# Kernel optimization log

Measured on AMD Instinct MI355X. Metric: run time of the kernel, lower is better.

The kernel has to match this reference:

```python
import jax, jax.numpy as jnp
import numpy as np

N_NODES = 50000
N_EDGES = 600000
D_IN = 128
HID = 128
N_SAGE = 2          # num_layers - 1
N_GRAPHS = 512
BN_EPS = 1e-5


def setup_inputs() -> dict:
    key = jax.random.key(0)
    ks = jax.random.split(key, 12)
    s = 1.0 / np.sqrt(HID)
    x = jax.random.normal(ks[0], (N_NODES, D_IN), dtype=jnp.float32)
    edge_index = jax.random.randint(ks[1], (2, N_EDGES), 0, N_NODES, dtype=jnp.int32)
    batch = jnp.sort(jax.random.randint(ks[2], (N_NODES,), 0, N_GRAPHS, dtype=jnp.int32))
    # GIN MLP: Linear(D_IN,HID) -> ReLU -> Linear(HID,HID)
    gin_w1 = jax.random.normal(ks[3], (D_IN, HID), dtype=jnp.float32) * s
    gin_b1 = jnp.zeros((HID,), jnp.float32)
    gin_w2 = jax.random.normal(ks[4], (HID, HID), dtype=jnp.float32) * s
    gin_b2 = jnp.zeros((HID,), jnp.float32)
    # SAGEConv layers: lin_l (neighbors, with bias), lin_r (root, no bias)
    sage_wl = jax.random.normal(ks[5], (N_SAGE, HID, HID), dtype=jnp.float32) * s
    sage_bl = jnp.zeros((N_SAGE, HID), jnp.float32)
    sage_wr = jax.random.normal(ks[6], (N_SAGE, HID, HID), dtype=jnp.float32) * s
    # BatchNorm per layer (3 layers)
    bn_gamma = jnp.ones((1 + N_SAGE, HID), jnp.float32)
    bn_beta = jnp.zeros((1 + N_SAGE, HID), jnp.float32)
    return {"x": x, "edge_index": edge_index, "batch": batch,
            "gin_w1": gin_w1, "gin_b1": gin_b1, "gin_w2": gin_w2, "gin_b2": gin_b2,
            "sage_wl": sage_wl, "sage_bl": sage_bl, "sage_wr": sage_wr,
            "bn_gamma": bn_gamma, "bn_beta": bn_beta}


def _batchnorm(h, gamma, beta):
    # training-mode BN over the node dimension (biased variance, as torch)
    mu = jnp.mean(h, axis=0)
    var = jnp.var(h, axis=0)
    return gamma * (h - mu) * jax.lax.rsqrt(var + BN_EPS) + beta


def reference(x, edge_index, batch, gin_w1, gin_b1, gin_w2, gin_b2,
              sage_wl, sage_bl, sage_wr, bn_gamma, bn_beta):
    n = x.shape[0]
    src, dst = edge_index[0], edge_index[1]

    # ---- Layer 0: GINConv (eps=0): mlp(x + sum_{j->i} x_j) ----
    agg = jax.ops.segment_sum(x[src], dst, num_segments=n)  # [N, D_IN]
    h = x + agg
    h = jax.nn.relu(h @ gin_w1 + gin_b1) @ gin_w2 + gin_b2
    h = jax.nn.relu(_batchnorm(h, bn_gamma[0], bn_beta[0]))
    # dropout is identity (eval mode)

    # degree for mean aggregation (shared across SAGE layers)
    deg = jax.ops.segment_sum(jnp.ones((src.shape[0],), h.dtype), dst, num_segments=n)
    inv_deg = (1.0 / jnp.maximum(deg, 1.0))[:, None]  # [N,1]

    # ---- SAGE layers: lin_l(mean_{j->i} h_j) + lin_r(h_i) ----
    for l in range(N_SAGE):
        neigh = jax.ops.segment_sum(h[src], dst, num_segments=n) * inv_deg
        h = neigh @ sage_wl[l] + sage_bl[l] + h @ sage_wr[l]
        h = jax.nn.relu(_batchnorm(h, bn_gamma[l + 1], bn_beta[l + 1]))

    # ---- global mean pool over batch ids ----
    sums = jax.ops.segment_sum(h, batch, num_segments=N_GRAPHS)  # [G, HID]
    counts = jax.ops.segment_sum(jnp.ones((n,), h.dtype), batch, num_segments=N_GRAPHS)
    return sums / jnp.maximum(counts, 1.0)[:, None]
```

## Files before the change

### kernel.cpp

```cpp
#include <hip/hip_runtime.h>

#define N_NODES 50000
#define N_EDGES 600000
#define HID 128
#define N_GRAPHS 512
#define BN_EPS 1e-5f
#define INV_N (1.0f / 50000.0f)

typedef __attribute__((ext_vector_type(8))) short bf16x8;
typedef __attribute__((ext_vector_type(4))) float f32x4;

__device__ __forceinline__ unsigned short f2b(float f) {
    unsigned u = __float_as_uint(f);
    return (unsigned short)((u + 0x7FFFu + ((u >> 16) & 1u)) >> 16);
}
__device__ __forceinline__ float b2f(unsigned short h) {
    return __uint_as_float(((unsigned)h) << 16);
}

#define CONVX_BLOCKS 6250
#define WCONV_BLOCKS 384
#define DEG_BLOCKS   2344
__global__ __launch_bounds__(256) void prep_kernel(
    const float* __restrict__ x, const float* __restrict__ gw1, const float* __restrict__ gw2,
    const float* __restrict__ swl, const float* __restrict__ swr, const int* __restrict__ dst,
    unsigned short* __restrict__ x16, unsigned short* __restrict__ wt, int* __restrict__ deg)
{
    int b = blockIdx.x;
    int t = threadIdx.x;
    if (b < CONVX_BLOCKS) {
        int gid = b * 256 + t;
        int i = gid >> 5, l = gid & 31;
        if (i >= N_NODES) return;
        int c0 = l * 4;
        float4 v = *(const float4*)(x + (size_t)i * 128 + c0);
        ushort4 o;
        o.x = f2b(v.x); o.y = f2b(v.y); o.z = f2b(v.z); o.w = f2b(v.w);
        *(ushort4*)(x16 + (size_t)i * 128 + c0) = o;
    } else if (b < CONVX_BLOCKS + WCONV_BLOCKS) {
        int gid = (b - CONVX_BLOCKS) * 256 + t;
        int m = gid >> 14;
        int e = gid & 16383;
        int k = e >> 7;
        int n = e & 127;
        const float* src = (m == 0) ? gw1 : (m == 1) ? gw2 : (m == 2) ? swl
                         : (m == 3) ? swr : (m == 4) ? (swl + 16384) : (swr + 16384);
        wt[m * 16384 + n * 128 + k] = f2b(src[k * 128 + n]);
    } else {
        int e = (b - CONVX_BLOCKS - WCONV_BLOCKS) * 256 + t;
        if (e < N_EDGES) atomicAdd(&deg[dst[e]], 1);
    }
}

#define ALLOC_BLOCKS 196
__global__ __launch_bounds__(256) void alloc_kernel(int* __restrict__ cursor,
                                                    int* __restrict__ row_beg,
                                                    float* __restrict__ inv_deg,
                                                    int* __restrict__ total,
                                                    const int* __restrict__ batch,
                                                    int* __restrict__ gstart) {
    if (blockIdx.x >= ALLOC_BLOCKS) {
        int g = (blockIdx.x - ALLOC_BLOCKS) * 256 + threadIdx.x;
        if (g > N_GRAPHS) return;
        int lo = 0, hi = N_NODES;
        while (lo < hi) {
            int mid = (lo + hi) >> 1;
            if (batch[mid] < g) lo = mid + 1; else hi = mid;
        }
        gstart[g] = lo;
        return;
    }
    __shared__ int tmp[256];
    __shared__ int base;
    int i = blockIdx.x * 256 + threadIdx.x;
    int d = (i < N_NODES) ? cursor[i] : 0;
    tmp[threadIdx.x] = d;
    __syncthreads();
#pragma unroll
    for (int off = 1; off < 256; off <<= 1) {
        int v = (threadIdx.x >= off) ? tmp[threadIdx.x - off] : 0;
        __syncthreads();
        tmp[threadIdx.x] += v;
        __syncthreads();
    }
    if (threadIdx.x == 255) base = atomicAdd(total, tmp[255]);
    __syncthreads();
    if (i < N_NODES) {
        int b = base + tmp[threadIdx.x] - d;
        row_beg[i] = b;
        cursor[i] = b;
        inv_deg[i] = 1.0f / fmaxf((float)d, 1.0f);
    }
}

__global__ void csr_fill_kernel(const int* __restrict__ src, const int* __restrict__ dst,
                                int* __restrict__ cursor, unsigned short* __restrict__ csr_src, int nE) {
    int e = blockIdx.x * blockDim.x + threadIdx.x;
    if (e < nE) {
        int pos = atomicAdd(&cursor[dst[e]], 1);
        csr_src[pos] = (unsigned short)src[e];
    }
}

#define IDXCAP 2048
template<bool AFF, bool MEAN, bool HACT>
__global__ __launch_bounds__(256) void aggregate_kernel(
    const unsigned short* __restrict__ feat,
    const int* __restrict__ row_beg, const int* __restrict__ row_end,
    const unsigned short* __restrict__ csr_src,
    const float* __restrict__ stats, const float* __restrict__ gamma,
    const float* __restrict__ beta, const float* __restrict__ inv_deg,
    unsigned short* __restrict__ agg, unsigned short* __restrict__ hact, int n)
{
    __shared__ unsigned short idxbuf[IDXCAP];
    const int t = threadIdx.x;
    const int node0 = blockIdx.x * 16;
    const int node = node0 + (t >> 4);
    const int lane = t & 15;
    const int c0 = lane * 8;

    const int last = (node0 + 15 < n) ? node0 + 15 : n - 1;
    const int ebeg = row_beg[node0];
    const int ecnt = row_end[last] - ebeg;
    const bool lds_ok = (ecnt <= IDXCAP);
    if (lds_ok) {
        for (int i = t; i < ecnt; i += 256) idxbuf[i] = csr_src[ebeg + i];
    }
    __syncthreads();
    if (node >= n) return;

    float cc[8], ss[8];
    if (AFF) {
#pragma unroll
        for (int j = 0; j < 8; j++) {
            int col = c0 + j;
            float mu = stats[col] * INV_N;
            float var = stats[128 + col] * INV_N - mu * mu;
            float rs = rsqrtf(var + BN_EPS);
            float c = gamma[col] * rs;
            cc[j] = c;
            ss[j] = beta[col] - mu * c;
        }
    }

    float a[8];
#pragma unroll
    for (int j = 0; j < 8; j++) a[j] = 0.f;

    const int beg = row_beg[node];
    const int deg = row_end[node] - beg;

    if (lds_ok) {
        const int off = beg - ebeg;
        int e = 0;
        for (; e + 7 < deg; e += 8) {
            int s[8];
#pragma unroll
            for (int u = 0; u < 8; u++) s[u] = idxbuf[off + e + u];
            bf16x8 v[8];
#pragma unroll
            for (int u = 0; u < 8; u++)
                v[u] = *(const bf16x8*)(feat + (size_t)s[u] * 128 + c0);
#pragma unroll
            for (int u = 0; u < 8; u++) {
#pragma unroll
                for (int j = 0; j < 8; j++) {
                    float tv = b2f((unsigned short)v[u][j]);
                    if (AFF) tv = fmaxf(tv * cc[j] + ss[j], 0.f);
                    a[j] += tv;
                }
            }
        }
        for (; e + 3 < deg; e += 4) {
            int s[4];
#pragma unroll
            for (int u = 0; u < 4; u++) s[u] = idxbuf[off + e + u];
            bf16x8 v[4];
#pragma unroll
            for (int u = 0; u < 4; u++)
                v[u] = *(const bf16x8*)(feat + (size_t)s[u] * 128 + c0);
#pragma unroll
            for (int u = 0; u < 4; u++) {
#pragma unroll
                for (int j = 0; j < 8; j++) {
                    float tv = b2f((unsigned short)v[u][j]);
                    if (AFF) tv = fmaxf(tv * cc[j] + ss[j], 0.f);
                    a[j] += tv;
                }
            }
        }
        for (; e < deg; e++) {
            int s0 = idxbuf[off + e];
            bf16x8 v0 = *(const bf16x8*)(feat + (size_t)s0 * 128 + c0);
#pragma unroll
            for (int j = 0; j < 8; j++) {
                float tv = b2f((unsigned short)v0[j]);
                if (AFF) tv = fmaxf(tv * cc[j] + ss[j], 0.f);
                a[j] += tv;
            }
        }
    } else {
        int e = beg, end = beg + deg;
        for (; e + 3 < end; e += 4) {
            int s0 = csr_src[e];
            int s1 = csr_src[e + 1];
            int s2 = csr_src[e + 2];
            int s3 = csr_src[e + 3];
            bf16x8 v0 = *(const bf16x8*)(feat + (size_t)s0 * 128 + c0);
            bf16x8 v1 = *(const bf16x8*)(feat + (size_t)s1 * 128 + c0);
            bf16x8 v2 = *(const bf16x8*)(feat + (size_t)s2 * 128 + c0);
            bf16x8 v3 = *(const bf16x8*)(feat + (size_t)s3 * 128 + c0);
#pragma unroll
            for (int j = 0; j < 8; j++) {
                float t0 = b2f((unsigned short)v0[j]);
                float t1 = b2f((unsigned short)v1[j]);
                float t2 = b2f((unsigned short)v2[j]);
                float t3 = b2f((unsigned short)v3[j]);
                if (AFF) {
                    t0 = fmaxf(t0 * cc[j] + ss[j], 0.f);
                    t1 = fmaxf(t1 * cc[j] + ss[j], 0.f);
                    t2 = fmaxf(t2 * cc[j] + ss[j], 0.f);
                    t3 = fmaxf(t3 * cc[j] + ss[j], 0.f);
                }
                a[j] += (t0 + t1) + (t2 + t3);
            }
        }
        for (; e < end; e++) {
            int s0 = csr_src[e];
            bf16x8 v0 = *(const bf16x8*)(feat + (size_t)s0 * 128 + c0);
#pragma unroll
            for (int j = 0; j < 8; j++) {
                float t0 = b2f((unsigned short)v0[j]);
                if (AFF) t0 = fmaxf(t0 * cc[j] + ss[j], 0.f);
                a[j] += t0;
            }
        }
    }

    if (MEAN) {
        float s = inv_deg[node];
#pragma unroll
        for (int j = 0; j < 8; j++) a[j] *= s;
    }
    bf16x8 o;
#pragma unroll
    for (int j = 0; j < 8; j++) o[j] = (short)f2b(a[j]);
    *(bf16x8*)(agg + (size_t)node * 128 + c0) = o;

    if (HACT) {
        bf16x8 v = *(const bf16x8*)(feat + (size_t)node * 128 + c0);
        bf16x8 h;
#pragma unroll
        for (int j = 0; j < 8; j++)
            h[j] = (short)f2b(fmaxf(b2f((unsigned short)v[j]) * cc[j] + ss[j], 0.f));
        *(bf16x8*)(hact + (size_t)node * 128 + c0) = h;
    }
}

__global__ __launch_bounds__(256, 2) void gemm_gin_kernel(
    const unsigned short* __restrict__ X, const unsigned short* __restrict__ AGG,
    const unsigned short* __restrict__ W1t, const unsigned short* __restrict__ W2t,
    const float* __restrict__ b1, const float* __restrict__ b2,
    float* __restrict__ stats, unsigned short* __restrict__ Cb,
    int M, int ntiles)
{
    __shared__ unsigned short t1[32][136];
    __shared__ float red[2][128];

    const int t = threadIdx.x;
    const int wave = t >> 6;
    const int lane = t & 63;
    const int colhalf = wave & 1;
    const int rowpair = wave >> 1;
    const int m16 = lane & 15;
    const int quad = lane >> 4;
    const int k0 = quad * 8;
    const int colbase = colhalf * 64;
    const int lrow = rowpair * 16 + m16;

    const bf16x8 zero8 = {0, 0, 0, 0, 0, 0, 0, 0};

    bf16x8 w1f[4][4], w2f[4][4];
#pragma unroll
    for (int ct = 0; ct < 4; ct++) {
        int col = colbase + ct * 16 + m16;
#pragma unroll
        for (int kc = 0; kc < 4; kc++) {
            w1f[ct][kc] = *(const bf16x8*)(W1t + (size_t)col * 128 + kc * 32 + k0);
            w2f[ct][kc] = *(const bf16x8*)(W2t + (size_t)col * 128 + kc * 32 + k0);
        }
    }
    f32x4 bs1[4], bs2[4];
#pragma unroll
    for (int ct = 0; ct < 4; ct++) {
        bs1[ct] = *(const f32x4*)(b1 + colbase + ct * 16 + quad * 4);
        bs2[ct] = *(const f32x4*)(b2 + colbase + ct * 16 + quad * 4);
    }

    float psum[4][4], psq[4][4];
#pragma unroll
    for (int ct = 0; ct < 4; ct++)
#pragma unroll
        for (int r = 0; r < 4; r++) { psum[ct][r] = 0.f; psq[ct][r] = 0.f; }

    for (int tile = blockIdx.x; tile < ntiles; tile += gridDim.x) {
        int arow = tile * 32 + rowpair * 16 + m16;
        bool aok = arow < M;

        bf16x8 a[4];
#pragma unroll
        for (int kc = 0; kc < 4; kc++) {
            if (aok) {
                bf16x8 vx = *(const bf16x8*)(X + (size_t)arow * 128 + kc * 32 + k0);
                bf16x8 vg = *(const bf16x8*)(AGG + (size_t)arow * 128 + kc * 32 + k0);
                bf16x8 r;
#pragma unroll
                for (int i = 0; i < 8; i++)
                    r[i] = (short)f2b(b2f((unsigned short)vx[i]) + b2f((unsigned short)vg[i]));
                a[kc] = r;
            } else {
                a[kc] = zero8;
            }
        }

        f32x4 acc[4];
#pragma unroll
        for (int ct = 0; ct < 4; ct++) acc[ct] = (f32x4){0.f, 0.f, 0.f, 0.f};
#pragma unroll
        for (int kc = 0; kc < 4; kc++)
#pragma unroll
            for (int ct = 0; ct < 4; ct++)
                acc[ct] = __builtin_amdgcn_mfma_f32_16x16x32_bf16(w1f[ct][kc], a[kc], acc[ct], 0, 0, 0);

        __syncthreads();
#pragma unroll
        for (int ct = 0; ct < 4; ct++) {
            f32x4 v = acc[ct] + bs1[ct];
            ushort4 o;
            o.x = f2b(fmaxf(v[0], 0.f));
            o.y = f2b(fmaxf(v[1], 0.f));
            o.z = f2b(fmaxf(v[2], 0.f));
            o.w = f2b(fmaxf(v[3], 0.f));
            *(ushort4*)&t1[lrow][colbase + ct * 16 + quad * 4] = o;
        }
        __syncthreads();

        bf16x8 ta[4];
#pragma unroll
        for (int kc = 0; kc < 4; kc++)
            ta[kc] = *(const bf16x8*)&t1[lrow][kc * 32 + k0];

        f32x4 acc2[4];
#pragma unroll
        for (int ct = 0; ct < 4; ct++) acc2[ct] = (f32x4){0.f, 0.f, 0.f, 0.f};
#pragma unroll
        for (int kc = 0; kc < 4; kc++)
#pragma unroll
            for (int ct = 0; ct < 4; ct++)
                acc2[ct] = __builtin_amdgcn_mfma_f32_16x16x32_bf16(w2f[ct][kc], ta[kc], acc2[ct], 0, 0, 0);

        int orow = arow;
        if (orow < M) {
#pragma unroll
            for (int ct = 0; ct < 4; ct++) {
                f32x4 v = acc2[ct] + bs2[ct];
                int col = colbase + ct * 16 + quad * 4;
#pragma unroll
                for (int r = 0; r < 4; r++) { psum[ct][r] += v[r]; psq[ct][r] += v[r] * v[r]; }
                ushort4 o;
                o.x = f2b(v[0]); o.y = f2b(v[1]); o.z = f2b(v[2]); o.w = f2b(v[3]);
                *(ushort4*)(Cb + (size_t)orow * 128 + col) = o;
            }
        }
    }

#pragma unroll
    for (int ct = 0; ct < 4; ct++)
#pragma unroll
        for (int r = 0; r < 4; r++) {
#pragma unroll
            for (int mask = 1; mask <= 8; mask <<= 1) {
                psum[ct][r] += __shfl_xor(psum[ct][r], mask, 64);
                psq[ct][r]  += __shfl_xor(psq[ct][r], mask, 64);
            }
        }
    __syncthreads();
    if (m16 == 0) {
#pragma unroll
        for (int ct = 0; ct < 4; ct++)
#pragma unroll
            for (int r = 0; r < 4; r++)
                red[rowpair][colbase + ct * 16 + quad * 4 + r] = psum[ct][r];
    }
    __syncthreads();
    if (t < 128) atomicAdd(&stats[t], red[0][t] + red[1][t]);
    __syncthreads();
    if (m16 == 0) {
#pragma unroll
        for (int ct = 0; ct < 4; ct++)
#pragma unroll
            for (int r = 0; r < 4; r++)
                red[rowpair][colbase + ct * 16 + quad * 4 + r] = psq[ct][r];
    }
    __syncthreads();
    if (t < 128) atomicAdd(&stats[128 + t], red[0][t] + red[1][t]);
}

__global__ __launch_bounds__(256) void gemm_dual_kernel(
    const unsigned short* __restrict__ A1, const unsigned short* __restrict__ A2,
    const unsigned short* __restrict__ W1t, const unsigned short* __restrict__ W2t,
    const float* __restrict__ bias, float* __restrict__ stats,
    unsigned short* __restrict__ Cb, int M, int ntiles)
{
    __shared__ float red[128];

    const int t = threadIdx.x;
    const int wave = t >> 6;
    const int lane = t & 63;
    const int m16 = lane & 15;
    const int quad = lane >> 4;
    const int k0 = quad * 8;
    const int colbase = wave * 32;

    const bf16x8 zero8 = {0, 0, 0, 0, 0, 0, 0, 0};

    bf16x8 w1f[2][4], w2f[2][4];
#pragma unroll
    for (int ct = 0; ct < 2; ct++) {
        int col = colbase + ct * 16 + m16;
#pragma unroll
        for (int kc = 0; kc < 4; kc++) {
            w1f[ct][kc] = *(const bf16x8*)(W1t + (size_t)col * 128 + kc * 32 + k0);
            w2f[ct][kc] = *(const bf16x8*)(W2t + (size_t)col * 128 + kc * 32 + k0);
        }
    }
    f32x4 bs[2];
#pragma unroll
    for (int ct = 0; ct < 2; ct++)
        bs[ct] = *(const f32x4*)(bias + colbase + ct * 16 + quad * 4);

    float psum[2][4], psq[2][4];
#pragma unroll
    for (int ct = 0; ct < 2; ct++)
#pragma unroll
        for (int r = 0; r < 4; r++) { psum[ct][r] = 0.f; psq[ct][r] = 0.f; }

    bf16x8 a1[4], a2[4], a1n[4], a2n[4];

    int tile = blockIdx.x;
    if (tile < ntiles) {
        int arow = tile * 16 + m16;
        bool aok = arow < M;
#pragma unroll
        for (int kc = 0; kc < 4; kc++) {
            a1[kc] = aok ? *(const bf16x8*)(A1 + (size_t)arow * 128 + kc * 32 + k0) : zero8;
            a2[kc] = aok ? *(const bf16x8*)(A2 + (size_t)arow * 128 + kc * 32 + k0) : zero8;
        }
    }

    for (; tile < ntiles; tile += gridDim.x) {
        int nt = tile + gridDim.x;
        if (nt < ntiles) {
            int arow = nt * 16 + m16;
            bool aok = arow < M;
#pragma unroll
            for (int kc = 0; kc < 4; kc++) {
                a1n[kc] = aok ? *(const bf16x8*)(A1 + (size_t)arow * 128 + kc * 32 + k0) : zero8;
                a2n[kc] = aok ? *(const bf16x8*)(A2 + (size_t)arow * 128 + kc * 32 + k0) : zero8;
            }
        }

        f32x4 acc[2];
        acc[0] = (f32x4){0.f, 0.f, 0.f, 0.f};
        acc[1] = (f32x4){0.f, 0.f, 0.f, 0.f};
#pragma unroll
        for (int kc = 0; kc < 4; kc++) {
#pragma unroll
            for (int ct = 0; ct < 2; ct++) {
                acc[ct] = __builtin_amdgcn_mfma_f32_16x16x32_bf16(w1f[ct][kc], a1[kc], acc[ct], 0, 0, 0);
                acc[ct] = __builtin_amdgcn_mfma_f32_16x16x32_bf16(w2f[ct][kc], a2[kc], acc[ct], 0, 0, 0);
            }
        }

        int orow = tile * 16 + m16;
        if (orow < M) {
#pragma unroll
            for (int ct = 0; ct < 2; ct++) {
                f32x4 v = acc[ct] + bs[ct];
                int col = colbase + ct * 16 + quad * 4;
#pragma unroll
                for (int r = 0; r < 4; r++) { psum[ct][r] += v[r]; psq[ct][r] += v[r] * v[r]; }
                ushort4 o;
                o.x = f2b(v[0]); o.y = f2b(v[1]); o.z = f2b(v[2]); o.w = f2b(v[3]);
                *(ushort4*)(Cb + (size_t)orow * 128 + col) = o;
            }
        }

        if (nt < ntiles) {
            a1[0] = a1n[0]; a1[1] = a1n[1]; a1[2] = a1n[2]; a1[3] = a1n[3];
            a2[0] = a2n[0]; a2[1] = a2n[1]; a2[2] = a2n[2]; a2[3] = a2n[3];
        }
    }

#pragma unroll
    for (int ct = 0; ct < 2; ct++)
#pragma unroll
        for (int r = 0; r < 4; r++) {
#pragma unroll
            for (int mask = 1; mask <= 8; mask <<= 1) {
                psum[ct][r] += __shfl_xor(psum[ct][r], mask, 64);
                psq[ct][r]  += __shfl_xor(psq[ct][r], mask, 64);
            }
        }
    if (m16 == 0) {
#pragma unroll
        for (int ct = 0; ct < 2; ct++)
#pragma unroll
            for (int r = 0; r < 4; r++)
                red[colbase + ct * 16 + quad * 4 + r] = psum[ct][r];
    }
    __syncthreads();
    if (t < 128) atomicAdd(&stats[t], red[t]);
    __syncthreads();
    if (m16 == 0) {
#pragma unroll
        for (int ct = 0; ct < 2; ct++)
#pragma unroll
            for (int r = 0; r < 4; r++)
                red[colbase + ct * 16 + quad * 4 + r] = psq[ct][r];
    }
    __syncthreads();
    if (t < 128) atomicAdd(&stats[128 + t], red[t]);
}

__global__ __launch_bounds__(128) void pool_mean_kernel(const unsigned short* __restrict__ h,
                                                        const int* __restrict__ gstart,
                                                        const float* __restrict__ stats,
                                                        const float* __restrict__ gamma,
                                                        const float* __restrict__ beta,
                                                        float* __restrict__ out) {
    __shared__ float red[8][128];
    int g = blockIdx.x;
    int t = threadIdx.x;
    int lane = t & 15, grp = t >> 4;
    int c0 = lane * 8;
    float c[8], b[8];
#pragma unroll
    for (int j = 0; j < 8; j++) {
        int col = c0 + j;
        float mu = stats[col] * INV_N;
        float var = stats[128 + col] * INV_N - mu * mu;
        float rs = rsqrtf(var + BN_EPS);
        c[j] = gamma[col] * rs;
        b[j] = beta[col] - mu * c[j];
    }
    int beg = gstart[g];
    int end = gstart[g + 1];
    float s[8];
#pragma unroll
    for (int j = 0; j < 8; j++) s[j] = 0.f;
    for (int i = beg + grp; i < end; i += 8) {
        bf16x8 v = *(const bf16x8*)(h + (size_t)i * 128 + c0);
#pragma unroll
        for (int j = 0; j < 8; j++)
            s[j] += fmaxf(b2f((unsigned short)v[j]) * c[j] + b[j], 0.f);
    }
#pragma unroll
    for (int j = 0; j < 8; j++) red[grp][c0 + j] = s[j];
    __syncthreads();
    if (t < 16) {
        float cnt = fmaxf((float)(end - beg), 1.0f);
        int cc0 = t * 8;
#pragma unroll
        for (int j = 0; j < 8; j++) {
            float tot = 0.f;
#pragma unroll
            for (int r = 0; r < 8; r++) tot += red[r][cc0 + j];
            out[(size_t)g * 128 + cc0 + j] = tot / cnt;
        }
    }
}

extern "C" void kernel_launch(void* const* d_in, const int* in_sizes, int n_in,
                              void* d_out, int out_size, void* d_ws, size_t ws_size,
                              hipStream_t stream) {
    const float* x    = (const float*)d_in[0];
    const int*   ei   = (const int*)d_in[1];
    const int*   src  = ei;
    const int*   dst  = ei + N_EDGES;
    const int*   batch = (const int*)d_in[2];
    const float* gw1  = (const float*)d_in[3];
    const float* gb1  = (const float*)d_in[4];
    const float* gw2  = (const float*)d_in[5];
    const float* gb2  = (const float*)d_in[6];
    const float* swl  = (const float*)d_in[7];
    const float* sbl  = (const float*)d_in[8];
    const float* swr  = (const float*)d_in[9];
    const float* bng  = (const float*)d_in[10];
    const float* bnb  = (const float*)d_in[11];
    float* out = (float*)d_out;

    float* ws = (float*)d_ws;
    unsigned short* x16    = (unsigned short*)(ws + 0);
    unsigned short* agg16  = (unsigned short*)(ws + 3200000);
    unsigned short* hact16 = (unsigned short*)(ws + 6400000);
    unsigned short* hpre16 = (unsigned short*)(ws + 9600000);
    unsigned short* wt     = (unsigned short*)(ws + 12800000);
    float*          inv_deg= ws + 12850000;
    int*            row_beg= (int*)(ws + 12900000);
    int*            cursor = (int*)(ws + 12950000);
    int*            total  = cursor + 50000;
    float*          stats  = (float*)(cursor + 50001);
    unsigned short* csr_src= (unsigned short*)(ws + 13100000);
    int*            gstart = (int*)(ws + 13700000);

    const int aggr_blocks = (N_NODES + 15) / 16;
    const int ntiles32 = (N_NODES + 31) / 32;
    const int ntiles16 = (N_NODES + 15) / 16;
    const int ggrid = 512;

    hipMemsetAsync(cursor, 0, (50001 + 768) * sizeof(int), stream);

    prep_kernel<<<CONVX_BLOCKS + WCONV_BLOCKS + DEG_BLOCKS, 256, 0, stream>>>(
        x, gw1, gw2, swl, swr, dst, x16, wt, cursor);

    alloc_kernel<<<ALLOC_BLOCKS + 3, 256, 0, stream>>>(cursor, row_beg, inv_deg, total, batch, gstart);
    csr_fill_kernel<<<(N_EDGES + 255) / 256, 256, 0, stream>>>(src, dst, cursor, csr_src, N_EDGES);

    aggregate_kernel<false, false, false><<<aggr_blocks, 256, 0, stream>>>(
        x16, row_beg, cursor, csr_src, nullptr, nullptr, nullptr, nullptr, agg16, nullptr, N_NODES);
    gemm_gin_kernel<<<ggrid, 256, 0, stream>>>(
        x16, agg16, wt + 0 * 16384, wt + 1 * 16384, gb1, gb2, stats + 0, hpre16, N_NODES, ntiles32);

    aggregate_kernel<true, true, true><<<aggr_blocks, 256, 0, stream>>>(
        hpre16, row_beg, cursor, csr_src, stats + 0, bng + 0 * HID, bnb + 0 * HID, inv_deg,
        agg16, hact16, N_NODES);
    gemm_dual_kernel<<<ggrid, 256, 0, stream>>>(
        agg16, hact16, wt + 2 * 16384, wt + 3 * 16384, sbl + 0 * HID, stats + 256, hpre16, N_NODES, ntiles16);

    aggregate_kernel<true, true, true><<<aggr_blocks, 256, 0, stream>>>(
        hpre16, row_beg, cursor, csr_src, stats + 256, bng + 1 * HID, bnb + 1 * HID, inv_deg,
        agg16, hact16, N_NODES);
    gemm_dual_kernel<<<ggrid, 256, 0, stream>>>(
        agg16, hact16, wt + 4 * 16384, wt + 5 * 16384, sbl + 1 * HID, stats + 512, hpre16, N_NODES, ntiles16);

    pool_mean_kernel<<<N_GRAPHS, 128, 0, stream>>>(
        hpre16, gstart, stats + 512, bng + 2 * HID, bnb + 2 * HID, out);
}
```

Baseline: 348.9 us.

## Store features in column-sliced layout and gather per slice for cache locality

Feature matrices are rearranged into 8 column slices of 16 bf16 each (slice-major), and the aggregation becomes a per-slice gather kernel so each block's working set (one 1.6MB slice) fits in L2. BN+ReLU application is moved out of the gather into a separate elementwise finish kernel that writes activated features once. BN stats atomics are spread across 8 partial copies to reduce contention. This adds two extra kernel launches and an extra full read/write pass per layer in exchange for better gather cache reuse.

```diff
diff --git a/kernel.cpp b/kernel.cpp
--- a/kernel.cpp
+++ b/kernel.cpp
@@ -6,6 +6,9 @@
 #define N_GRAPHS 512
 #define BN_EPS 1e-5f
 #define INV_N (1.0f / 50000.0f)
+#define SLICE_STRIDE 800000
+#define GATHER_GROUPS 391
+#define IDXCAP 4096
 
 typedef __attribute__((ext_vector_type(8))) short bf16x8;
 typedef __attribute__((ext_vector_type(4))) float f32x4;
@@ -16,6 +19,13 @@
 }
 __device__ __forceinline__ float b2f(unsigned short h) {
     return __uint_as_float(((unsigned)h) << 16);
+}
+
+__device__ __forceinline__ float stats_sum(const float* __restrict__ s, int idx) {
+    float v = 0.f;
+#pragma unroll
+    for (int r = 0; r < 8; r++) v += s[r * 256 + idx];
+    return v;
 }
 
 #define CONVX_BLOCKS 6250
@@ -36,7 +46,7 @@
         float4 v = *(const float4*)(x + (size_t)i * 128 + c0);
         ushort4 o;
         o.x = f2b(v.x); o.y = f2b(v.y); o.z = f2b(v.z); o.w = f2b(v.w);
-        *(ushort4*)(x16 + (size_t)i * 128 + c0) = o;
+        *(ushort4*)(x16 + (size_t)(l >> 2) * SLICE_STRIDE + (size_t)i * 16 + (l & 3) * 4) = o;
     } else if (b < CONVX_BLOCKS + WCONV_BLOCKS) {
         int gid = (b - CONVX_BLOCKS) * 256 + t;
         int m = gid >> 14;
@@ -102,53 +112,38 @@
     }
 }
 
-#define IDXCAP 2048
-template<bool AFF, bool MEAN, bool HACT>
-__global__ __launch_bounds__(256) void aggregate_kernel(
-    const unsigned short* __restrict__ feat,
+template<bool MEAN>
+__global__ __launch_bounds__(256) void gather_slice_kernel(
+    const unsigned short* __restrict__ feat_s,
     const int* __restrict__ row_beg, const int* __restrict__ row_end,
     const unsigned short* __restrict__ csr_src,
-    const float* __restrict__ stats, const float* __restrict__ gamma,
-    const float* __restrict__ beta, const float* __restrict__ inv_deg,
-    unsigned short* __restrict__ agg, unsigned short* __restrict__ hact, int n)
+    const float* __restrict__ inv_deg,
+    unsigned short* __restrict__ out_s)
 {
     __shared__ unsigned short idxbuf[IDXCAP];
     const int t = threadIdx.x;
-    const int node0 = blockIdx.x * 16;
-    const int node = node0 + (t >> 4);
-    const int lane = t & 15;
-    const int c0 = lane * 8;
-
-    const int last = (node0 + 15 < n) ? node0 + 15 : n - 1;
+    const int slice = blockIdx.x & 7;
+    const int grp = blockIdx.x >> 3;
+    const int node0 = grp * 128;
+    const int nlast = (node0 + 127 < N_NODES) ? node0 + 127 : N_NODES - 1;
+    const int node = node0 + (t >> 1);
+    const int l8 = (t & 1) * 8;
+    const unsigned short* fbase = feat_s + (size_t)slice * SLICE_STRIDE + l8;
+
     const int ebeg = row_beg[node0];
-    const int ecnt = row_end[last] - ebeg;
+    const int ecnt = row_end[nlast] - ebeg;
     const bool lds_ok = (ecnt <= IDXCAP);
-    if (lds_ok) {
+    if (lds_ok)
         for (int i = t; i < ecnt; i += 256) idxbuf[i] = csr_src[ebeg + i];
-    }
-    __syncthreads();
-    if (node >= n) return;
-
-    float cc[8], ss[8];
-    if (AFF) {
-#pragma unroll
-        for (int j = 0; j < 8; j++) {
-            int col = c0 + j;
-            float mu = stats[col] * INV_N;
-            float var = stats[128 + col] * INV_N - mu * mu;
-            float rs = rsqrtf(var + BN_EPS);
-            float c = gamma[col] * rs;
-            cc[j] = c;
-            ss[j] = beta[col] - mu * c;
-        }
-    }
-
-    float a[8];
-#pragma unroll
-    for (int j = 0; j < 8; j++) a[j] = 0.f;
+    __syncthreads();
+    if (node >= N_NODES) return;
 
     const int beg = row_beg[node];
     const int deg = row_end[node] - beg;
+
+    float a[8];
+#pragma unroll
+    for (int j = 0; j < 8; j++) a[j] = 0.f;
 
     if (lds_ok) {
         const int off = beg - ebeg;
@@ -160,16 +155,12 @@
             bf16x8 v[8];
 #pragma unroll
             for (int u = 0; u < 8; u++)
-                v[u] = *(const bf16x8*)(feat + (size_t)s[u] * 128 + c0);
-#pragma unroll
-            for (int u = 0; u < 8; u++) {
-#pragma unroll
-                for (int j = 0; j < 8; j++) {
-                    float tv = b2f((unsigned short)v[u][j]);
-                    if (AFF) tv = fmaxf(tv * cc[j] + ss[j], 0.f);
-                    a[j] += tv;
-                }
-            }
+                v[u] = *(const bf16x8*)(fbase + (size_t)s[u] * 16);
+#pragma unroll
+            for (int u = 0; u < 8; u++)
+#pragma unroll
+                for (int j = 0; j < 8; j++)
+                    a[j] += b2f((unsigned short)v[u][j]);
         }
         for (; e + 3 < deg; e += 4) {
             int s[4];
@@ -178,83 +169,39 @@
             bf16x8 v[4];
 #pragma unroll
             for (int u = 0; u < 4; u++)
-                v[u] = *(const bf16x8*)(feat + (size_t)s[u] * 128 + c0);
-#pragma unroll
-            for (int u = 0; u < 4; u++) {
-#pragma unroll
-                for (int j = 0; j < 8; j++) {
-                    float tv = b2f((unsigned short)v[u][j]);
-                    if (AFF) tv = fmaxf(tv * cc[j] + ss[j], 0.f);
-                    a[j] += tv;
-                }
-            }
+                v[u] = *(const bf16x8*)(fbase + (size_t)s[u] * 16);
+#pragma unroll
+            for (int u = 0; u < 4; u++)
+#pragma unroll
+                for (int j = 0; j < 8; j++)
+                    a[j] += b2f((unsigned short)v[u][j]);
         }
         for (; e < deg; e++) {
             int s0 = idxbuf[off + e];
-            bf16x8 v0 = *(const bf16x8*)(feat + (size_t)s0 * 128 + c0);
-#pragma unroll
-            for (int j = 0; j < 8; j++) {
-                float tv = b2f((unsigned short)v0[j]);
-                if (AFF) tv = fmaxf(tv * cc[j] + ss[j], 0.f);
-                a[j] += tv;
-            }
+            bf16x8 v0 = *(const bf16x8*)(fbase + (size_t)s0 * 16);
+#pragma unroll
+            for (int j = 0; j < 8; j++)
+                a[j] += b2f((unsigned short)v0[j]);
         }
     } else {
-        int e = beg, end = beg + deg;
-        for (; e + 3 < end; e += 4) {
+        for (int e = beg; e < beg + deg; e++) {
             int s0 = csr_src[e];
-            int s1 = csr_src[e + 1];
-            int s2 = csr_src[e + 2];
-            int s3 = csr_src[e + 3];
-            bf16x8 v0 = *(const bf16x8*)(feat + (size_t)s0 * 128 + c0);
-            bf16x8 v1 = *(const bf16x8*)(feat + (size_t)s1 * 128 + c0);
-            bf16x8 v2 = *(const bf16x8*)(feat + (size_t)s2 * 128 + c0);
-            bf16x8 v3 = *(const bf16x8*)(feat + (size_t)s3 * 128 + c0);
-#pragma unroll
-            for (int j = 0; j < 8; j++) {
-                float t0 = b2f((unsigned short)v0[j]);
-                float t1 = b2f((unsigned short)v1[j]);
-                float t2 = b2f((unsigned short)v2[j]);
-                float t3 = b2f((unsigned short)v3[j]);
-                if (AFF) {
-                    t0 = fmaxf(t0 * cc[j] + ss[j], 0.f);
-                    t1 = fmaxf(t1 * cc[j] + ss[j], 0.f);
-                    t2 = fmaxf(t2 * cc[j] + ss[j], 0.f);
-                    t3 = fmaxf(t3 * cc[j] + ss[j], 0.f);
-                }
-                a[j] += (t0 + t1) + (t2 + t3);
-            }
-        }
-        for (; e < end; e++) {
-            int s0 = csr_src[e];
-            bf16x8 v0 = *(const bf16x8*)(feat + (size_t)s0 * 128 + c0);
-#pragma unroll
-            for (int j = 0; j < 8; j++) {
-                float t0 = b2f((unsigned short)v0[j]);
-                if (AFF) t0 = fmaxf(t0 * cc[j] + ss[j], 0.f);
-                a[j] += t0;
-            }
+            bf16x8 v0 = *(const bf16x8*)(fbase + (size_t)s0 * 16);
+#pragma unroll
+            for (int j = 0; j < 8; j++)
+                a[j] += b2f((unsigned short)v0[j]);
         }
     }
 
     if (MEAN) {
-        float s = inv_deg[node];
-#pragma unroll
-        for (int j = 0; j < 8; j++) a[j] *= s;
+        float sc = inv_deg[node];
+#pragma unroll
+        for (int j = 0; j < 8; j++) a[j] *= sc;
     }
     bf16x8 o;
 #pragma unroll
     for (int j = 0; j < 8; j++) o[j] = (short)f2b(a[j]);
-    *(bf16x8*)(agg + (size_t)node * 128 + c0) = o;
-
-    if (HACT) {
-        bf16x8 v = *(const bf16x8*)(feat + (size_t)node * 128 + c0);
-        bf16x8 h;
-#pragma unroll
-        for (int j = 0; j < 8; j++)
-            h[j] = (short)f2b(fmaxf(b2f((unsigned short)v[j]) * cc[j] + ss[j], 0.f));
-        *(bf16x8*)(hact + (size_t)node * 128 + c0) = h;
-    }
+    *(bf16x8*)(out_s + (size_t)slice * SLICE_STRIDE + (size_t)node * 16 + l8) = o;
 }
 
 __global__ __launch_bounds__(256, 2) void gemm_gin_kernel(
@@ -311,8 +258,10 @@
 #pragma unroll
         for (int kc = 0; kc < 4; kc++) {
             if (aok) {
-                bf16x8 vx = *(const bf16x8*)(X + (size_t)arow * 128 + kc * 32 + k0);
-                bf16x8 vg = *(const bf16x8*)(AGG + (size_t)arow * 128 + kc * 32 + k0);
+                size_t aoff = (size_t)(kc * 2 + (quad >> 1)) * SLICE_STRIDE
+                            + (size_t)arow * 16 + (quad & 1) * 8;
+                bf16x8 vx = *(const bf16x8*)(X + aoff);
+                bf16x8 vg = *(const bf16x8*)(AGG + aoff);
                 bf16x8 r;
 #pragma unroll
                 for (int i = 0; i < 8; i++)
@@ -359,17 +308,16 @@
             for (int ct = 0; ct < 4; ct++)
                 acc2[ct] = __builtin_amdgcn_mfma_f32_16x16x32_bf16(w2f[ct][kc], ta[kc], acc2[ct], 0, 0, 0);
 
-        int orow = arow;
-        if (orow < M) {
+        if (arow < M) {
 #pragma unroll
             for (int ct = 0; ct < 4; ct++) {
                 f32x4 v = acc2[ct] + bs2[ct];
-                int col = colbase + ct * 16 + quad * 4;
 #pragma unroll
                 for (int r = 0; r < 4; r++) { psum[ct][r] += v[r]; psq[ct][r] += v[r] * v[r]; }
                 ushort4 o;
                 o.x = f2b(v[0]); o.y = f2b(v[1]); o.z = f2b(v[2]); o.w = f2b(v[3]);
-                *(ushort4*)(Cb + (size_t)orow * 128 + col) = o;
+                int cs = (colbase >> 4) + ct;
+                *(ushort4*)(Cb + (size_t)cs * SLICE_STRIDE + (size_t)arow * 16 + quad * 4) = o;
             }
         }
     }
@@ -393,7 +341,7 @@
                 red[rowpair][colbase + ct * 16 + quad * 4 + r] = psum[ct][r];
     }
     __syncthreads();
-    if (t < 128) atomicAdd(&stats[t], red[0][t] + red[1][t]);
+    if (t < 128) atomicAdd(&stats[(blockIdx.x & 7) * 256 + t], red[0][t] + red[1][t]);
     __syncthreads();
     if (m16 == 0) {
 #pragma unroll
@@ -403,7 +351,7 @@
                 red[rowpair][colbase + ct * 16 + quad * 4 + r] = psq[ct][r];
     }
     __syncthreads();
-    if (t < 128) atomicAdd(&stats[128 + t], red[0][t] + red[1][t]);
+    if (t < 128) atomicAdd(&stats[(blockIdx.x & 7) * 256 + 128 + t], red[0][t] + red[1][t]);
 }
 
 __global__ __launch_bounds__(256) void gemm_dual_kernel(
@@ -453,8 +401,10 @@
         bool aok = arow < M;
 #pragma unroll
         for (int kc = 0; kc < 4; kc++) {
-            a1[kc] = aok ? *(const bf16x8*)(A1 + (size_t)arow * 128 + kc * 32 + k0) : zero8;
-            a2[kc] = aok ? *(const bf16x8*)(A2 + (size_t)arow * 128 + kc * 32 + k0) : zero8;
+            size_t aoff = (size_t)(kc * 2 + (quad >> 1)) * SLICE_STRIDE
+                        + (size_t)arow * 16 + (quad & 1) * 8;
+            a1[kc] = aok ? *(const bf16x8*)(A1 + aoff) : zero8;
+            a2[kc] = aok ? *(const bf16x8*)(A2 + aoff) : zero8;
         }
     }
 
@@ -465,8 +415,10 @@
             bool aok = arow < M;
 #pragma unroll
             for (int kc = 0; kc < 4; kc++) {
-                a1n[kc] = aok ? *(const bf16x8*)(A1 + (size_t)arow * 128 + kc * 32 + k0) : zero8;
-                a2n[kc] = aok ? *(const bf16x8*)(A2 + (size_t)arow * 128 + kc * 32 + k0) : zero8;
+                size_t aoff = (size_t)(kc * 2 + (quad >> 1)) * SLICE_STRIDE
+                            + (size_t)arow * 16 + (quad & 1) * 8;
+                a1n[kc] = aok ? *(const bf16x8*)(A1 + aoff) : zero8;
+                a2n[kc] = aok ? *(const bf16x8*)(A2 + aoff) : zero8;
             }
         }
 
@@ -487,12 +439,12 @@
 #pragma unroll
             for (int ct = 0; ct < 2; ct++) {
                 f32x4 v = acc[ct] + bs[ct];
-                int col = colbase + ct * 16 + quad * 4;
 #pragma unroll
                 for (int r = 0; r < 4; r++) { psum[ct][r] += v[r]; psq[ct][r] += v[r] * v[r]; }
                 ushort4 o;
                 o.x = f2b(v[0]); o.y = f2b(v[1]); o.z = f2b(v[2]); o.w = f2b(v[3]);
-                *(ushort4*)(Cb + (size_t)orow * 128 + col) = o;
+                int cs = wave * 2 + ct;
+                *(ushort4*)(Cb + (size_t)cs * SLICE_STRIDE + (size_t)orow * 16 + quad * 4) = o;
             }
         }
 
@@ -520,7 +472,7 @@
                 red[colbase + ct * 16 + quad * 4 + r] = psum[ct][r];
     }
     __syncthreads();
-    if (t < 128) atomicAdd(&stats[t], red[t]);
+    if (t < 128) atomicAdd(&stats[(blockIdx.x & 7) * 256 + t], red[t]);
     __syncthreads();
     if (m16 == 0) {
 #pragma unroll
@@ -530,54 +482,82 @@
                 red[colbase + ct * 16 + quad * 4 + r] = psq[ct][r];
     }
     __syncthreads();
-    if (t < 128) atomicAdd(&stats[128 + t], red[t]);
-}
-
-__global__ __launch_bounds__(128) void pool_mean_kernel(const unsigned short* __restrict__ h,
+    if (t < 128) atomicAdd(&stats[(blockIdx.x & 7) * 256 + 128 + t], red[t]);
+}
+
+__global__ __launch_bounds__(256) void finish_kernel(
+    const unsigned short* __restrict__ Hpre, const float* __restrict__ stats,
+    const float* __restrict__ gamma, const float* __restrict__ beta,
+    unsigned short* __restrict__ Hact)
+{
+    __shared__ float cs[2][128];
+    int t = threadIdx.x;
+    if (t < 128) {
+        float mu = stats_sum(stats, t) * INV_N;
+        float var = stats_sum(stats, 128 + t) * INV_N - mu * mu;
+        float rs = rsqrtf(var + BN_EPS);
+        float c = gamma[t] * rs;
+        cs[0][t] = c;
+        cs[1][t] = beta[t] - mu * c;
+    }
+    __syncthreads();
+    int gid = blockIdx.x * 256 + t;
+    int e0 = gid * 8;
+    int s = (unsigned)e0 / SLICE_STRIDE;
+    int rem = e0 - s * SLICE_STRIDE;
+    int col0 = s * 16 + (rem & 15);
+    bf16x8 v = *(const bf16x8*)(Hpre + e0);
+    bf16x8 o;
+#pragma unroll
+    for (int j = 0; j < 8; j++)
+        o[j] = (short)f2b(fmaxf(b2f((unsigned short)v[j]) * cs[0][col0 + j] + cs[1][col0 + j], 0.f));
+    *(bf16x8*)(Hact + e0) = o;
+}
+
+__global__ __launch_bounds__(256) void pool_mean_kernel(const unsigned short* __restrict__ h_s,
                                                         const int* __restrict__ gstart,
                                                         const float* __restrict__ stats,
                                                         const float* __restrict__ gamma,
                                                         const float* __restrict__ beta,
                                                         float* __restrict__ out) {
-    __shared__ float red[8][128];
+    __shared__ float red[16][128];
     int g = blockIdx.x;
     int t = threadIdx.x;
-    int lane = t & 15, grp = t >> 4;
-    int c0 = lane * 8;
+    int grp = t >> 4;
+    int ci = t & 15;
+    int s = ci >> 1, off = (ci & 1) * 8;
+    int c0 = ci * 8;
     float c[8], b[8];
 #pragma unroll
     for (int j = 0; j < 8; j++) {
         int col = c0 + j;
-        float mu = stats[col] * INV_N;
-        float var = stats[128 + col] * INV_N - mu * mu;
+        float mu = stats_sum(stats, col) * INV_N;
+        float var = stats_sum(stats, 128 + col) * INV_N - mu * mu;
         float rs = rsqrtf(var + BN_EPS);
         c[j] = gamma[col] * rs;
         b[j] = beta[col] - mu * c[j];
     }
     int beg = gstart[g];
     int end = gstart[g + 1];
-    float s[8];
-#pragma unroll
-    for (int j = 0; j < 8; j++) s[j] = 0.f;
-    for (int i = beg + grp; i < end; i += 8) {
-        bf16x8 v = *(const bf16x8*)(h + (size_t)i * 128 + c0);
+    float sa[8];
+#pragma unroll
+    for (int j = 0; j < 8; j++) sa[j] = 0.f;
+    const unsigned short* base = h_s + (size_t)s * SLICE_STRIDE + off;
+    for (int i = beg + grp; i < end; i += 16) {
+        bf16x8 v = *(const bf16x8*)(base + (size_t)i * 16);
 #pragma unroll
         for (int j = 0; j < 8; j++)
-            s[j] += fmaxf(b2f((unsigned short)v[j]) * c[j] + b[j], 0.f);
-    }
-#pragma unroll
-    for (int j = 0; j < 8; j++) red[grp][c0 + j] = s[j];
-    __syncthreads();
-    if (t < 16) {
+            sa[j] += fmaxf(b2f((unsigned short)v[j]) * c[j] + b[j], 0.f);
+    }
+#pragma unroll
+    for (int j = 0; j < 8; j++) red[grp][c0 + j] = sa[j];
+    __syncthreads();
+    if (t < 128) {
         float cnt = fmaxf((float)(end - beg), 1.0f);
-        int cc0 = t * 8;
-#pragma unroll
-        for (int j = 0; j < 8; j++) {
-            float tot = 0.f;
-#pragma unroll
-            for (int r = 0; r < 8; r++) tot += red[r][cc0 + j];
-            out[(size_t)g * 128 + cc0 + j] = tot / cnt;
-        }
+        float tot = 0.f;
+#pragma unroll
+        for (int r = 0; r < 16; r++) tot += red[r][t];
+        out[(size_t)g * 128 + t] = tot / cnt;
     }
 }
 
@@ -601,10 +581,10 @@
     float* out = (float*)d_out;
 
     float* ws = (float*)d_ws;
-    unsigned short* x16    = (unsigned short*)(ws + 0);
-    unsigned short* agg16  = (unsigned short*)(ws + 3200000);
-    unsigned short* hact16 = (unsigned short*)(ws + 6400000);
-    unsigned short* hpre16 = (unsigned short*)(ws + 9600000);
+    unsigned short* x16_s  = (unsigned short*)(ws + 0);
+    unsigned short* agg_s  = (unsigned short*)(ws + 3200000);
+    unsigned short* hact_s = (unsigned short*)(ws + 6400000);
+    unsigned short* hpre_s = (unsigned short*)(ws + 9600000);
     unsigned short* wt     = (unsigned short*)(ws + 12800000);
     float*          inv_deg= ws + 12850000;
     int*            row_beg= (int*)(ws + 12900000);
@@ -614,36 +594,41 @@
     unsigned short* csr_src= (unsigned short*)(ws + 13100000);
     int*            gstart = (int*)(ws + 13700000);
 
-    const int aggr_blocks = (N_NODES + 15) / 16;
+    const int ggrid = 512;
     const int ntiles32 = (N_NODES + 31) / 32;
     const int ntiles16 = (N_NODES + 15) / 16;
-    const int ggrid = 512;
-
-    hipMemsetAsync(cursor, 0, (50001 + 768) * sizeof(int), stream);
+    const int gather_grid = GATHER_GROUPS * 8;
+
+    hipMemsetAsync(cursor, 0, (50001 + 3 * 8 * 256) * sizeof(int), stream);
 
     prep_kernel<<<CONVX_BLOCKS + WCONV_BLOCKS + DEG_BLOCKS, 256, 0, stream>>>(
-        x, gw1, gw2, swl, swr, dst, x16, wt, cursor);
+        x, gw1, gw2, swl, swr, dst, x16_s, wt, cursor);
 
     alloc_kernel<<<ALLOC_BLOCKS + 3, 256, 0, stream>>>(cursor, row_beg, inv_deg, total, batch, gstart);
     csr_fill_kernel<<<(N_EDGES + 255) / 256, 256, 0, stream>>>(src, dst, cursor, csr_src, N_EDGES);
 
-    aggregate_kernel<false, false, false><<<aggr_blocks, 256, 0, stream>>>(
-        x16, row_beg, cursor, csr_src, nullptr, nullptr, nullptr, nullptr, agg16, nullptr, N_NODES);
+    gather_slice_kernel<false><<<gather_grid, 256, 0, stream>>>(
+        x16_s, row_beg, cursor, csr_src, nullptr, agg_s);
     gemm_gin_kernel<<<ggrid, 256, 0, stream>>>(
-        x16, agg16, wt + 0 * 16384, wt + 1 * 16384, gb1, gb2, stats + 0, hpre16, N_NODES, ntiles32);
-
-    aggregate_kernel<true, true, true><<<aggr_blocks, 256, 0, stream>>>(
-        hpre16, row_beg, cursor, csr_src, stats + 0, bng + 0 * HID, bnb + 0 * HID, inv_deg,
-        agg16, hact16, N_NODES);
+        x16_s, agg_s, wt + 0 * 16384, wt + 1 * 16384, gb1, gb2,
+        stats + 0 * 2048, hpre_s, N_NODES, ntiles32);
+    finish_kernel<<<3125, 256, 0, stream>>>(
+        hpre_s, stats + 0 * 2048, bng + 0 * HID, bnb + 0 * HID, hact_s);
+
+    gather_slice_kernel<true><<<gather_grid, 256, 0, stream>>>(
+        hact_s, row_beg, cursor, csr_src, inv_deg, agg_s);
     gemm_dual_kernel<<<ggrid, 256, 0, stream>>>(
-        agg16, hact16, wt + 2 * 16384, wt + 3 * 16384, sbl + 0 * HID, stats + 256, hpre16, N_NODES, ntiles16);
-
-    aggregate_kernel<true, true, true><<<aggr_blocks, 256, 0, stream>>>(
-        hpre16, row_beg, cursor, csr_src, stats + 256, bng + 1 * HID, bnb + 1 * HID, inv_deg,
-        agg16, hact16, N_NODES);
+        agg_s, hact_s, wt + 2 * 16384, wt + 3 * 16384, sbl + 0 * HID,
+        stats + 1 * 2048, hpre_s, N_NODES, ntiles16);
+    finish_kernel<<<3125, 256, 0, stream>>>(
+        hpre_s, stats + 1 * 2048, bng + 1 * HID, bnb + 1 * HID, hact_s);
+
+    gather_slice_kernel<true><<<gather_grid, 256, 0, stream>>>(
+        hact_s, row_beg, cursor, csr_src, inv_deg, agg_s);
     gemm_dual_kernel<<<ggrid, 256, 0, stream>>>(
-        agg16, hact16, wt + 4 * 16384, wt + 5 * 16384, sbl + 1 * HID, stats + 512, hpre16, N_NODES, ntiles16);
-
-    pool_mean_kernel<<<N_GRAPHS, 128, 0, stream>>>(
-        hpre16, gstart, stats + 512, bng + 2 * HID, bnb + 2 * HID, out);
-}
+        agg_s, hact_s, wt + 4 * 16384, wt + 5 * 16384, sbl + 1 * HID,
+        stats + 2 * 2048, hpre_s, N_NODES, ntiles16);
+
+    pool_mean_kernel<<<N_GRAPHS, 256, 0, stream>>>(
+        hpre_s, gstart, stats + 2 * 2048, bng + 2 * HID, bnb + 2 * HID, out);
+}
```

Result: faster. 312.4 us (-10.5%).
